# Kernel tuning notes

Measured on AMD Instinct MI355X. Metric: run time of the kernel, lower is better.

Reference implementation:

```python
import jax, jax.numpy as jnp
import numpy as np

H, D = 6, 64          # num_heads, head_dim (embed_dim = 384)
WIN = 33              # window_size
PAD = (WIN - 1) // 2  # 16


def setup_inputs() -> dict:
    key = jax.random.key(0)
    ks = jax.random.split(key, 9)
    B, L, E = 8, 1025, 384
    s = 1.0 / np.sqrt(E).astype(np.float32)
    return {
        "x": jax.random.normal(ks[0], (B, L, E), jnp.float32),
        "Wq": jax.random.normal(ks[1], (E, E), jnp.float32) * s,
        "bq": jax.random.normal(ks[2], (E,), jnp.float32) * 0.01,
        "Wk": jax.random.normal(ks[3], (E, E), jnp.float32) * s,
        "bk": jax.random.normal(ks[4], (E,), jnp.float32) * 0.01,
        "Wv": jax.random.normal(ks[5], (E, E), jnp.float32) * s,
        "bv": jax.random.normal(ks[6], (E,), jnp.float32) * 0.01,
        "Wo": jax.random.normal(ks[7], (E, E), jnp.float32) * s,
        "bo": jax.random.normal(ks[8], (E,), jnp.float32) * 0.01,
    }


def reference(x, Wq, bq, Wk, bk, Wv, bv, Wo, bo):
    B, L, E = x.shape
    scale = 1.0 / np.sqrt(D).astype(np.float32)

    def proj(W, b):
        # (B,L,E) -> (B,H,L,D)
        return (x @ W + b).reshape(B, L, H, D).transpose(0, 2, 1, 3)

    Q, K, V = proj(Wq, bq), proj(Wk, bk), proj(Wv, bv)

    # --- cls token (position 0): full attention over all keys ---
    s_cls = jnp.einsum('bhqd,bhkd->bhqk', Q[:, :, :1], K) * scale
    out_cls = jnp.einsum('bhqk,bhkd->bhqd', jax.nn.softmax(s_cls, -1), V)

    # --- remaining tokens: local window + cls appended to every window ---
    Lr = L - 1
    pos = jnp.arange(1, L)                                    # absolute query pos (Lr,)
    idx = pos[:, None] + jnp.arange(WIN)[None, :] - PAD
    # original masks out-of-range AND the cls slot (abs pos 0) inside the window
    valid = (idx >= 1) & (idx < L)
    idxc = jnp.clip(idx, 0, L - 1)

    Kw = K[:, :, idxc]
    Vw = V[:, :, idxc]
    cls_k = jnp.broadcast_to(K[:, :, :1, None, :], (B, H, Lr, 1, D))
    cls_v = jnp.broadcast_to(V[:, :, :1, None, :], (B, H, Lr, 1, D))
    Kw = jnp.concatenate([Kw, cls_k], axis=3)
    Vw = jnp.concatenate([Vw, cls_v], axis=3)
    mask = jnp.concatenate([valid, jnp.ones((Lr, 1), bool)], axis=-1)

    s_rest = jnp.einsum('bhld,bhlwd->bhlw', Q[:, :, 1:], Kw) * scale
    s_rest = jnp.where(mask[None, None], s_rest, -jnp.inf)
    a_rest = jax.nn.softmax(s_rest, axis=-1)
    out_rest = jnp.einsum('bhlw,bhlwd->bhld', a_rest, Vw)

    out = jnp.concatenate([out_cls, out_rest], axis=2)        # (B,H,L,D)
    out = out.transpose(0, 2, 1, 3).reshape(B, L, E)
    return out @ Wo + bo
```

## Files before the change

### kernel.cpp

```cpp
#include <hip/hip_runtime.h>
#include <hip/hip_bf16.h>

typedef unsigned short ushort_t;
typedef __attribute__((ext_vector_type(8))) short short8;
typedef __attribute__((ext_vector_type(4))) float f32x4;

constexpr int Bc = 8;
constexpr int Lc = 1025;
constexpr int Ec = 384;
constexpr int Hc = 6;
constexpr int Dc = 64;
constexpr int MT = Bc * Lc;
constexpr int BHLD = Bc * Hc * Lc * Dc;
constexpr int LT = 1032;
constexpr float SCALE = 0.125f;
constexpr int NCH = 5;

__device__ __forceinline__ float bf2f(ushort_t u) {
    union { unsigned int u; float f; } v; v.u = ((unsigned int)u) << 16; return v.f;
}
__device__ __forceinline__ ushort_t f2bf(float f) {
    union { float f; unsigned int u; } v; v.f = f;
    unsigned int r = v.u + 0x7FFFu + ((v.u >> 16) & 1u);
    return (ushort_t)(r >> 16);
}

#define GLOAD_LDS16(gp, lp)                                                          \
    __builtin_amdgcn_global_load_lds(                                                \
        (const __attribute__((address_space(1))) unsigned int*)(gp),                 \
        (__attribute__((address_space(3))) unsigned int*)(lp), 16, 0, 0)

__global__ __launch_bounds__(256) void cast_x_kernel(
    const float* __restrict__ x, ushort_t* __restrict__ xb)
{
    int i = blockIdx.x * 256 + threadIdx.x;
    float4 v = ((const float4*)x)[i];
    ushort4 o;
    o.x = f2bf(v.x); o.y = f2bf(v.y); o.z = f2bf(v.z); o.w = f2bf(v.w);
    ((ushort4*)xb)[i] = o;
}

__global__ __launch_bounds__(256) void castT_w_kernel(
    const float* __restrict__ Wq, const float* __restrict__ Wk,
    const float* __restrict__ Wv, const float* __restrict__ Wo,
    ushort_t* __restrict__ Wt_all)
{
    __shared__ float t[32][33];
    const int z = blockIdx.z;
    const float* W = (z == 0) ? Wq : (z == 1) ? Wk : (z == 2) ? Wv : Wo;
    ushort_t* Wt = Wt_all + (size_t)z * Ec * Ec;
    const int x0 = blockIdx.x * 32, y0 = blockIdx.y * 32;
    const int tx = threadIdx.x & 31, ty = threadIdx.x >> 5;
#pragma unroll
    for (int j = 0; j < 4; j++)
        t[ty + 8 * j][tx] = W[(size_t)(y0 + ty + 8 * j) * Ec + x0 + tx];
    __syncthreads();
#pragma unroll
    for (int j = 0; j < 4; j++)
        Wt[(size_t)(x0 + ty + 8 * j) * Ec + y0 + tx] = f2bf(t[tx][ty + 8 * j]);
}

__global__ __launch_bounds__(256) void qkv_mfma_kernel(
    const ushort_t* __restrict__ xb, const ushort_t* __restrict__ Wt,
    const float* __restrict__ bq, const float* __restrict__ bk,
    const float* __restrict__ bv, ushort_t* __restrict__ qkv)
{
    __shared__ __align__(16) ushort_t As[128 * 64];
    __shared__ __align__(16) ushort_t Bs[128 * 64];

    const int tid = threadIdx.x;
    const int lane = tid & 63;
    const int wid = tid >> 6;
    const int wr = wid >> 1, wc = wid & 1;
    const int m0 = blockIdx.x * 128;
    const int n0 = blockIdx.y * 128;
    const int which = n0 / Ec;
    const int nm0 = n0 - which * Ec;
    const ushort_t* Wmat = Wt + (size_t)which * Ec * Ec;
    const float* bias = (which == 0) ? bq : (which == 1) ? bk : bv;

    f32x4 acc[4][4];
#pragma unroll
    for (int i = 0; i < 4; i++)
#pragma unroll
        for (int j = 0; j < 4; j++) acc[i][j] = (f32x4){0.f, 0.f, 0.f, 0.f};

    for (int kt = 0; kt < Ec; kt += 64) {
#pragma unroll
        for (int c = 0; c < 4; c++) {
            int ci  = (wid * 4 + c) * 64 + lane;
            int row = ci >> 3, kc = ci & 7;
            int kcs = kc ^ (row & 7);
            int rowA = m0 + row; rowA = rowA < MT ? rowA : MT - 1;
            GLOAD_LDS16(xb + (size_t)rowA * Ec + kt + kcs * 8,
                        As + (size_t)(wid * 4 + c) * 512);
            GLOAD_LDS16(Wmat + (size_t)(nm0 + row) * Ec + kt + kcs * 8,
                        Bs + (size_t)(wid * 4 + c) * 512);
        }
        __syncthreads();

#pragma unroll
        for (int ki = 0; ki < 2; ki++) {
            short8 a[4], b[4];
            const int kchunk = ki * 4 + (lane >> 4);
#pragma unroll
            for (int mi = 0; mi < 4; mi++) {
                int row = wr * 64 + mi * 16 + (lane & 15);
                a[mi] = *(const short8*)(As + row * 64 + ((kchunk ^ (row & 7)) * 8));
            }
#pragma unroll
            for (int ni = 0; ni < 4; ni++) {
                int row = wc * 64 + ni * 16 + (lane & 15);
                b[ni] = *(const short8*)(Bs + row * 64 + ((kchunk ^ (row & 7)) * 8));
            }
#pragma unroll
            for (int mi = 0; mi < 4; mi++)
#pragma unroll
                for (int ni = 0; ni < 4; ni++)
                    acc[mi][ni] = __builtin_amdgcn_mfma_f32_16x16x32_bf16(
                        a[mi], b[ni], acc[mi][ni], 0, 0, 0);
        }
        __syncthreads();
    }

    const int colL = lane & 15;
    const int rowL = (lane >> 4) * 4;
#pragma unroll
    for (int ni = 0; ni < 4; ni++) {
        int nm = nm0 + wc * 64 + ni * 16 + colL;
        float bv_ = bias[nm];
        int h = nm >> 6, d = nm & 63;
#pragma unroll
        for (int mi = 0; mi < 4; mi++) {
#pragma unroll
            for (int r = 0; r < 4; r++) {
                int m = m0 + wr * 64 + mi * 16 + rowL + r;
                if (m < MT) {
                    int b_ = m / Lc, l = m - b_ * Lc;
                    qkv[(size_t)which * BHLD +
                        ((size_t)(b_ * Hc + h) * Lc + l) * Dc + d] =
                        f2bf(acc[mi][ni][r] + bv_);
                }
            }
        }
    }
}

__global__ __launch_bounds__(256) void vT_kernel(
    const ushort_t* __restrict__ qkv, ushort_t* __restrict__ vt)
{
    __shared__ ushort_t t[64][68];
    const int bh = blockIdx.y;
    const int l0 = blockIdx.x * 64;
    const ushort_t* V = qkv + 2 * (size_t)BHLD + (size_t)bh * Lc * Dc;
    ushort_t* vto = vt + (size_t)bh * 64 * LT;
    const int tid = threadIdx.x;
#pragma unroll
    for (int i = 0; i < 4; i++) {
        int idx = tid + i * 256;
        int l = idx >> 4, dc = idx & 15;
        int ls = l0 + l; ls = ls > 1024 ? 1024 : ls;
        ushort4 v = *(const ushort4*)(V + (size_t)ls * Dc + dc * 4);
        *(ushort4*)&t[l][dc * 4] = v;
    }
    __syncthreads();
#pragma unroll
    for (int i = 0; i < 4; i++) {
        int idx = tid + i * 256;
        int d = idx >> 4, lc = idx & 15;
        ushort4 o;
        o.x = t[lc * 4 + 0][d]; o.y = t[lc * 4 + 1][d];
        o.z = t[lc * 4 + 2][d]; o.w = t[lc * 4 + 3][d];
        int lw = l0 + lc * 4;
        if (lw <= 1024)
            *(ushort4*)(vto + (size_t)d * LT + lw) = o;
    }
}

__global__ __launch_bounds__(256) void cls_part_kernel(
    const ushort_t* __restrict__ qkv, float* __restrict__ part)
{
    const int bh = blockIdx.x, ch = blockIdx.y;
    const int base = ch * 256;
    const int count = min(256, Lc - base);
    const ushort_t* Q = qkv + (size_t)bh * Lc * Dc;
    const ushort_t* K = Q + (size_t)BHLD;
    const ushort_t* V = Q + 2 * (size_t)BHLD;

    __shared__ float qs[64];
    __shared__ float ps[256];
    __shared__ float red[256];

    const int tid = threadIdx.x;
    if (tid < 64) qs[tid] = bf2f(Q[tid]);
    __syncthreads();

    float s = -1e30f;
    if (tid < count) {
        const ushort4* kp = (const ushort4*)(K + (size_t)(base + tid) * Dc);
        float acc = 0.f;
#pragma unroll
        for (int c = 0; c < 16; c++) {
            ushort4 kv = kp[c];
            acc += qs[c * 4 + 0] * bf2f(kv.x) + qs[c * 4 + 1] * bf2f(kv.y) +
                   qs[c * 4 + 2] * bf2f(kv.z) + qs[c * 4 + 3] * bf2f(kv.w);
        }
        s = acc * SCALE;
    }
    red[tid] = s; __syncthreads();
    for (int off = 128; off > 0; off >>= 1) {
        if (tid < off) red[tid] = fmaxf(red[tid], red[tid + off]);
        __syncthreads();
    }
    const float m = red[0];
    __syncthreads();

    float p = (tid < count) ? __expf(s - m) : 0.f;
    ps[tid] = p;
    red[tid] = p; __syncthreads();
    for (int off = 128; off > 0; off >>= 1) {
        if (tid < off) red[tid] += red[tid + off];
        __syncthreads();
    }
    const float S = red[0];
    __syncthreads();

    const int d = tid & 63, sl = tid >> 6;
    float acc = 0.f;
    for (int i = sl; i < count; i += 4)
        acc += ps[i] * bf2f(V[(size_t)(base + i) * Dc + d]);
    red[tid] = acc; __syncthreads();
    if (tid < 64) {
        float o = red[tid] + red[tid + 64] + red[tid + 128] + red[tid + 192];
        float* pp = part + (size_t)(bh * NCH + ch) * 66;
        pp[2 + tid] = o;
        if (tid == 0) { pp[0] = m; pp[1] = S; }
    }
}

__global__ __launch_bounds__(64) void cls_comb_kernel(
    const float* __restrict__ part, ushort_t* __restrict__ attnb)
{
    const int bh = blockIdx.x, d = threadIdx.x;
    float M = -1e30f;
#pragma unroll
    for (int ch = 0; ch < NCH; ch++)
        M = fmaxf(M, part[(size_t)(bh * NCH + ch) * 66]);
    float S = 0.f, O = 0.f;
#pragma unroll
    for (int ch = 0; ch < NCH; ch++) {
        const float* pp = part + (size_t)(bh * NCH + ch) * 66;
        float w = __expf(pp[0] - M);
        S += pp[1] * w;
        O += pp[2 + d] * w;
    }
    const int b_ = bh / Hc, h = bh - b_ * Hc;
    attnb[(size_t)(b_ * Lc) * Ec + h * 64 + d] = f2bf(O / S);
}

__global__ __launch_bounds__(256) void win_mfma_kernel(
    const ushort_t* __restrict__ qkv, const ushort_t* __restrict__ vt,
    ushort_t* __restrict__ attnb)
{
    __shared__ __align__(16) ushort_t Kb[128 * 64];
    __shared__ __align__(16) ushort_t Vb[64 * 128];
    __shared__ __align__(16) ushort_t QP[64 * 128];

    const int t = blockIdx.x, bh = blockIdx.y;
    const int l0 = 1 + t * 64, k0 = l0 - 17;
    const int tid = threadIdx.x, lane = tid & 63, wid = tid >> 6;
    const ushort_t* Qg = qkv + (size_t)bh * Lc * Dc;
    const ushort_t* Kg = Qg + (size_t)BHLD;
    const ushort_t* Vt = vt + (size_t)bh * 64 * LT;

#pragma unroll
    for (int i = 0; i < 4; i++) {
        int p = (i * 4 + wid) * 64 + lane;
        {
            int j = p >> 3, c = p & 7, g = c ^ (j & 7);
            int kp = (j <= 111) ? min(max(k0 + j, 0), 1024) : 0;
            GLOAD_LDS16(Kg + (size_t)kp * Dc + g * 8,
                        Kb + (size_t)(i * 4 + wid) * 512);
        }
        {
            int d = p >> 4, jc = p & 15, g = jc ^ (d & 15);
            int kb = (g <= 13) ? max(k0 + g * 8, 0) : 0;
            GLOAD_LDS16(Vt + (size_t)d * LT + kb,
                        Vb + (size_t)(i * 4 + wid) * 512);
        }
    }
#pragma unroll
    for (int i = 0; i < 2; i++) {
        int p = (i * 4 + wid) * 64 + lane;
        int q = p >> 3, c = p & 7, g = c ^ (q & 7);
        GLOAD_LDS16(Qg + (size_t)(l0 + q) * Dc + g * 8,
                    QP + (size_t)(i * 4 + wid) * 512);
    }
    __syncthreads();

    f32x4 sacc[8];
#pragma unroll
    for (int tj = 0; tj < 8; tj++) sacc[tj] = (f32x4){0.f, 0.f, 0.f, 0.f};
#pragma unroll
    for (int ki = 0; ki < 2; ki++) {
        const int gc = ki * 4 + (lane >> 4);
        const int qrow = wid * 16 + (lane & 15);
        short8 a = *(const short8*)(QP + qrow * 64 + ((gc ^ (qrow & 7)) * 8));
#pragma unroll
        for (int tj = 0; tj < 8; tj++) {
            int jrow = tj * 16 + (lane & 15);
            short8 b = *(const short8*)(Kb + jrow * 64 + ((gc ^ (jrow & 7)) * 8));
            sacc[tj] = __builtin_amdgcn_mfma_f32_16x16x32_bf16(a, b, sacc[tj], 0, 0, 0);
        }
    }
    __syncthreads();

    const int qb = wid * 16 + (lane >> 4) * 4;
    const int cl = lane & 15;
    float inv[4];
#pragma unroll
    for (int r = 0; r < 4; r++) {
        const int q = qb + r;
        float sv[8];
        float mx = -1e30f;
#pragma unroll
        for (int tj = 0; tj < 8; tj++) {
            int j = tj * 16 + cl;
            int kp = k0 + j;
            bool valid = (j == 112) ||
                         ((j >= q + 1) && (j <= q + 33) && (kp >= 1) && (kp <= 1024));
            float s = valid ? sacc[tj][r] * SCALE : -1e30f;
            sv[tj] = s;
            mx = fmaxf(mx, s);
        }
        mx = fmaxf(mx, __shfl_xor(mx, 1));
        mx = fmaxf(mx, __shfl_xor(mx, 2));
        mx = fmaxf(mx, __shfl_xor(mx, 4));
        mx = fmaxf(mx, __shfl_xor(mx, 8));
        float sum = 0.f;
#pragma unroll
        for (int tj = 0; tj < 8; tj++) {
            float pv = __expf(sv[tj] - mx);
            sv[tj] = pv;
            sum += pv;
        }
        sum += __shfl_xor(sum, 1);
        sum += __shfl_xor(sum, 2);
        sum += __shfl_xor(sum, 4);
        sum += __shfl_xor(sum, 8);
        inv[r] = 1.f / sum;
#pragma unroll
        for (int tj = 0; tj < 8; tj++) {
            int j = tj * 16 + cl;
            QP[q * 128 + (((j >> 3) ^ (q & 15)) * 8) + (j & 7)] = f2bf(sv[tj]);
        }
    }
    __syncthreads();

    f32x4 oacc[4];
#pragma unroll
    for (int dt = 0; dt < 4; dt++) oacc[dt] = (f32x4){0.f, 0.f, 0.f, 0.f};
#pragma unroll
    for (int kc = 0; kc < 4; kc++) {
        const int gc = kc * 4 + (lane >> 4);
        const int qrow = wid * 16 + (lane & 15);
        short8 pa = *(const short8*)(QP + qrow * 128 + ((gc ^ (qrow & 15)) * 8));
#pragma unroll
        for (int dt = 0; dt < 4; dt++) {
            int drow = dt * 16 + (lane & 15);
            short8 vb = *(const short8*)(Vb + drow * 128 + ((gc ^ (drow & 15)) * 8));
            oacc[dt] = __builtin_amdgcn_mfma_f32_16x16x32_bf16(pa, vb, oacc[dt], 0, 0, 0);
        }
    }

    const int b_ = bh / Hc, h = bh - b_ * Hc;
#pragma unroll
    for (int dt = 0; dt < 4; dt++) {
        int d = dt * 16 + cl;
#pragma unroll
        for (int r = 0; r < 4; r++) {
            int l = l0 + qb + r;
            attnb[(size_t)(b_ * Lc + l) * Ec + h * 64 + d] = f2bf(oacc[dt][r] * inv[r]);
        }
    }
}

__global__ __launch_bounds__(256) void out_mfma_kernel(
    const ushort_t* __restrict__ attn_rows, const ushort_t* __restrict__ Wot,
    const float* __restrict__ bo, float* __restrict__ out)
{
    __shared__ __align__(16) ushort_t As[128 * 64];
    __shared__ __align__(16) ushort_t Bs[128 * 64];

    const int tid = threadIdx.x;
    const int lane = tid & 63;
    const int wid = tid >> 6;
    const int wr = wid >> 1, wc = wid & 1;
    const int m0 = blockIdx.x * 128;
    const int n0 = blockIdx.y * 128;

    f32x4 acc[4][4];
#pragma unroll
    for (int i = 0; i < 4; i++)
#pragma unroll
        for (int j = 0; j < 4; j++) acc[i][j] = (f32x4){0.f, 0.f, 0.f, 0.f};

    for (int kt = 0; kt < Ec; kt += 64) {
#pragma unroll
        for (int c = 0; c < 4; c++) {
            int ci  = (wid * 4 + c) * 64 + lane;
            int row = ci >> 3, kc = ci & 7;
            int kcs = kc ^ (row & 7);
            int rowA = m0 + row; rowA = rowA < MT ? rowA : MT - 1;
            GLOAD_LDS16(attn_rows + (size_t)rowA * Ec + kt + kcs * 8,
                        As + (size_t)(wid * 4 + c) * 512);
            GLOAD_LDS16(Wot + (size_t)(n0 + row) * Ec + kt + kcs * 8,
                        Bs + (size_t)(wid * 4 + c) * 512);
        }
        __syncthreads();

#pragma unroll
        for (int ki = 0; ki < 2; ki++) {
            short8 a[4], b[4];
            const int kchunk = ki * 4 + (lane >> 4);
#pragma unroll
            for (int mi = 0; mi < 4; mi++) {
                int row = wr * 64 + mi * 16 + (lane & 15);
                a[mi] = *(const short8*)(As + row * 64 + ((kchunk ^ (row & 7)) * 8));
            }
#pragma unroll
            for (int ni = 0; ni < 4; ni++) {
                int row = wc * 64 + ni * 16 + (lane & 15);
                b[ni] = *(const short8*)(Bs + row * 64 + ((kchunk ^ (row & 7)) * 8));
            }
#pragma unroll
            for (int mi = 0; mi < 4; mi++)
#pragma unroll
                for (int ni = 0; ni < 4; ni++)
                    acc[mi][ni] = __builtin_amdgcn_mfma_f32_16x16x32_bf16(
                        a[mi], b[ni], acc[mi][ni], 0, 0, 0);
        }
        __syncthreads();
    }

    const int colL = lane & 15;
    const int rowL = (lane >> 4) * 4;
#pragma unroll
    for (int ni = 0; ni < 4; ni++) {
        int n = n0 + wc * 64 + ni * 16 + colL;
        float bo_v = bo[n];
#pragma unroll
        for (int mi = 0; mi < 4; mi++) {
#pragma unroll
            for (int r = 0; r < 4; r++) {
                int m = m0 + wr * 64 + mi * 16 + rowL + r;
                if (m < MT) out[(size_t)m * Ec + n] = acc[mi][ni][r] + bo_v;
            }
        }
    }
}

extern "C" void kernel_launch(void* const* d_in, const int* in_sizes, int n_in,
                              void* d_out, int out_size, void* d_ws, size_t ws_size,
                              hipStream_t stream)
{
    const float* x  = (const float*)d_in[0];
    const float* Wq = (const float*)d_in[1];
    const float* bq = (const float*)d_in[2];
    const float* Wk = (const float*)d_in[3];
    const float* bk = (const float*)d_in[4];
    const float* Wv = (const float*)d_in[5];
    const float* bv = (const float*)d_in[6];
    const float* Wo = (const float*)d_in[7];
    const float* bo = (const float*)d_in[8];
    float* out = (float*)d_out;

    ushort_t* xb    = (ushort_t*)d_ws;
    ushort_t* Wt    = xb + (size_t)MT * Ec;
    ushort_t* qkvb  = Wt + (size_t)4 * Ec * Ec;
    ushort_t* vtb   = qkvb + (size_t)3 * BHLD;
    ushort_t* attnb = vtb + (size_t)Bc * Hc * 64 * LT;
    float* clsp     = (float*)(attnb + (size_t)MT * Ec);

    cast_x_kernel<<<(MT * Ec) / 4 / 256, 256, 0, stream>>>(x, xb);
    castT_w_kernel<<<dim3(12, 12, 4), 256, 0, stream>>>(Wq, Wk, Wv, Wo, Wt);

    qkv_mfma_kernel<<<dim3((MT + 127) / 128, 9), 256, 0, stream>>>(
        xb, Wt, bq, bk, bv, qkvb);

    vT_kernel<<<dim3(17, Bc * Hc), 256, 0, stream>>>(qkvb, vtb);

    cls_part_kernel<<<dim3(Bc * Hc, NCH), 256, 0, stream>>>(qkvb, clsp);
    cls_comb_kernel<<<Bc * Hc, 64, 0, stream>>>(clsp, attnb);

    win_mfma_kernel<<<dim3(16, Bc * Hc), 256, 0, stream>>>(qkvb, vtb, attnb);

    out_mfma_kernel<<<dim3((MT + 127) / 128, 3), 256, 0, stream>>>(
        attnb, Wt + (size_t)3 * Ec * Ec, bo, out);
}
```

Before: 175.5 us.

## Fuse cast kernels, fold cls attention into window kernel, shrink output GEMM tile

Merges the x cast and weight transpose-cast into one prep launch. The two-stage cls attention (partial plus combine) becomes one extra block per head inside the window attention kernel, computed by a single block over all 1025 keys. The output projection GEMM M-tile drops from 128 to 64 rows, doubling block count for better occupancy on the large CU count. Together these cut three kernel launches, but the cls work is now a serial single-block tail per head.

```diff
diff --git a/kernel.cpp b/kernel.cpp
--- a/kernel.cpp
+++ b/kernel.cpp
@@ -14,7 +14,6 @@
 constexpr int BHLD = Bc * Hc * Lc * Dc;
 constexpr int LT = 1032;
 constexpr float SCALE = 0.125f;
-constexpr int NCH = 5;
 
 __device__ __forceinline__ float bf2f(ushort_t u) {
     union { unsigned int u; float f; } v; v.u = ((unsigned int)u) << 16; return v.f;
@@ -30,26 +29,28 @@
         (const __attribute__((address_space(1))) unsigned int*)(gp),                 \
         (__attribute__((address_space(3))) unsigned int*)(lp), 16, 0, 0)
 
-__global__ __launch_bounds__(256) void cast_x_kernel(
-    const float* __restrict__ x, ushort_t* __restrict__ xb)
-{
-    int i = blockIdx.x * 256 + threadIdx.x;
-    float4 v = ((const float4*)x)[i];
-    ushort4 o;
-    o.x = f2bf(v.x); o.y = f2bf(v.y); o.z = f2bf(v.z); o.w = f2bf(v.w);
-    ((ushort4*)xb)[i] = o;
-}
-
-__global__ __launch_bounds__(256) void castT_w_kernel(
+__global__ __launch_bounds__(256) void prep_kernel(
+    const float* __restrict__ x, ushort_t* __restrict__ xb,
     const float* __restrict__ Wq, const float* __restrict__ Wk,
     const float* __restrict__ Wv, const float* __restrict__ Wo,
     ushort_t* __restrict__ Wt_all)
 {
+    const int bid = blockIdx.x;
+    if (bid < 3075) {
+        int i = bid * 256 + threadIdx.x;
+        float4 v = ((const float4*)x)[i];
+        ushort4 o;
+        o.x = f2bf(v.x); o.y = f2bf(v.y); o.z = f2bf(v.z); o.w = f2bf(v.w);
+        ((ushort4*)xb)[i] = o;
+        return;
+    }
     __shared__ float t[32][33];
-    const int z = blockIdx.z;
+    const int b2 = bid - 3075;
+    const int z = b2 / 144, rem = b2 - z * 144;
+    const int yy = rem / 12, xx = rem - yy * 12;
     const float* W = (z == 0) ? Wq : (z == 1) ? Wk : (z == 2) ? Wv : Wo;
     ushort_t* Wt = Wt_all + (size_t)z * Ec * Ec;
-    const int x0 = blockIdx.x * 32, y0 = blockIdx.y * 32;
+    const int x0 = xx * 32, y0 = yy * 32;
     const int tx = threadIdx.x & 31, ty = threadIdx.x >> 5;
 #pragma unroll
     for (int j = 0; j < 4; j++)
@@ -177,88 +178,7 @@
     }
 }
 
-__global__ __launch_bounds__(256) void cls_part_kernel(
-    const ushort_t* __restrict__ qkv, float* __restrict__ part)
-{
-    const int bh = blockIdx.x, ch = blockIdx.y;
-    const int base = ch * 256;
-    const int count = min(256, Lc - base);
-    const ushort_t* Q = qkv + (size_t)bh * Lc * Dc;
-    const ushort_t* K = Q + (size_t)BHLD;
-    const ushort_t* V = Q + 2 * (size_t)BHLD;
-
-    __shared__ float qs[64];
-    __shared__ float ps[256];
-    __shared__ float red[256];
-
-    const int tid = threadIdx.x;
-    if (tid < 64) qs[tid] = bf2f(Q[tid]);
-    __syncthreads();
-
-    float s = -1e30f;
-    if (tid < count) {
-        const ushort4* kp = (const ushort4*)(K + (size_t)(base + tid) * Dc);
-        float acc = 0.f;
-#pragma unroll
-        for (int c = 0; c < 16; c++) {
-            ushort4 kv = kp[c];
-            acc += qs[c * 4 + 0] * bf2f(kv.x) + qs[c * 4 + 1] * bf2f(kv.y) +
-                   qs[c * 4 + 2] * bf2f(kv.z) + qs[c * 4 + 3] * bf2f(kv.w);
-        }
-        s = acc * SCALE;
-    }
-    red[tid] = s; __syncthreads();
-    for (int off = 128; off > 0; off >>= 1) {
-        if (tid < off) red[tid] = fmaxf(red[tid], red[tid + off]);
-        __syncthreads();
-    }
-    const float m = red[0];
-    __syncthreads();
-
-    float p = (tid < count) ? __expf(s - m) : 0.f;
-    ps[tid] = p;
-    red[tid] = p; __syncthreads();
-    for (int off = 128; off > 0; off >>= 1) {
-        if (tid < off) red[tid] += red[tid + off];
-        __syncthreads();
-    }
-    const float S = red[0];
-    __syncthreads();
-
-    const int d = tid & 63, sl = tid >> 6;
-    float acc = 0.f;
-    for (int i = sl; i < count; i += 4)
-        acc += ps[i] * bf2f(V[(size_t)(base + i) * Dc + d]);
-    red[tid] = acc; __syncthreads();
-    if (tid < 64) {
-        float o = red[tid] + red[tid + 64] + red[tid + 128] + red[tid + 192];
-        float* pp = part + (size_t)(bh * NCH + ch) * 66;
-        pp[2 + tid] = o;
-        if (tid == 0) { pp[0] = m; pp[1] = S; }
-    }
-}
-
-__global__ __launch_bounds__(64) void cls_comb_kernel(
-    const float* __restrict__ part, ushort_t* __restrict__ attnb)
-{
-    const int bh = blockIdx.x, d = threadIdx.x;
-    float M = -1e30f;
-#pragma unroll
-    for (int ch = 0; ch < NCH; ch++)
-        M = fmaxf(M, part[(size_t)(bh * NCH + ch) * 66]);
-    float S = 0.f, O = 0.f;
-#pragma unroll
-    for (int ch = 0; ch < NCH; ch++) {
-        const float* pp = part + (size_t)(bh * NCH + ch) * 66;
-        float w = __expf(pp[0] - M);
-        S += pp[1] * w;
-        O += pp[2 + d] * w;
-    }
-    const int b_ = bh / Hc, h = bh - b_ * Hc;
-    attnb[(size_t)(b_ * Lc) * Ec + h * 64 + d] = f2bf(O / S);
-}
-
-__global__ __launch_bounds__(256) void win_mfma_kernel(
+__global__ __launch_bounds__(256) void attn_kernel(
     const ushort_t* __restrict__ qkv, const ushort_t* __restrict__ vt,
     ushort_t* __restrict__ attnb)
 {
@@ -266,11 +186,71 @@
     __shared__ __align__(16) ushort_t Vb[64 * 128];
     __shared__ __align__(16) ushort_t QP[64 * 128];
 
-    const int t = blockIdx.x, bh = blockIdx.y;
-    const int l0 = 1 + t * 64, k0 = l0 - 17;
+    const int bh = blockIdx.y;
     const int tid = threadIdx.x, lane = tid & 63, wid = tid >> 6;
     const ushort_t* Qg = qkv + (size_t)bh * Lc * Dc;
     const ushort_t* Kg = Qg + (size_t)BHLD;
+    const int b_ = bh / Hc, h = bh - b_ * Hc;
+
+    if (blockIdx.x == 16) {
+        const ushort_t* Vg = Qg + 2 * (size_t)BHLD;
+        float* sc  = (float*)Kb;
+        float* red = (float*)Vb;
+
+        unsigned int qw = ((const unsigned int*)Qg)[lane & 31];
+        float qa = bf2f((ushort_t)(qw & 0xffff)), qb = bf2f((ushort_t)(qw >> 16));
+
+        float lmax = -1e30f;
+        for (int s = 0; s < 129; ++s) {
+            int k = s * 8 + wid * 2 + (lane >> 5);
+            bool ok = k < Lc;
+            int kc = ok ? k : 0;
+            unsigned int kw = ((const unsigned int*)(Kg + (size_t)kc * Dc))[lane & 31];
+            float p = qa * bf2f((ushort_t)(kw & 0xffff)) +
+                      qb * bf2f((ushort_t)(kw >> 16));
+            p += __shfl_xor(p, 1);  p += __shfl_xor(p, 2);
+            p += __shfl_xor(p, 4);  p += __shfl_xor(p, 8);
+            p += __shfl_xor(p, 16);
+            float s0 = p * SCALE;
+            if (ok && (lane & 31) == 0) sc[k] = s0;
+            float so = __shfl_xor(s0, 32);
+            int ko = s * 8 + wid * 2 + 1 - (lane >> 5);
+            if (!ok) s0 = -1e30f;
+            if (ko >= Lc) so = -1e30f;
+            lmax = fmaxf(lmax, fmaxf(s0, so));
+        }
+        if (lane == 0) red[wid] = lmax;
+        __syncthreads();
+        const float M = fmaxf(fmaxf(red[0], red[1]), fmaxf(red[2], red[3]));
+
+        float lsum = 0.f;
+        for (int k = tid; k < Lc; k += 256) {
+            float p = __expf(sc[k] - M);
+            sc[k] = p;
+            lsum += p;
+        }
+        lsum += __shfl_xor(lsum, 1);  lsum += __shfl_xor(lsum, 2);
+        lsum += __shfl_xor(lsum, 4);  lsum += __shfl_xor(lsum, 8);
+        lsum += __shfl_xor(lsum, 16); lsum += __shfl_xor(lsum, 32);
+        __syncthreads();
+        if (lane == 0) red[8 + wid] = lsum;
+        __syncthreads();
+        const float S = red[8] + red[9] + red[10] + red[11];
+
+        float acc = 0.f;
+        for (int k = wid; k < Lc; k += 4)
+            acc += sc[k] * bf2f(Vg[(size_t)k * Dc + lane]);
+        red[64 + wid * 64 + lane] = acc;
+        __syncthreads();
+        if (tid < 64) {
+            float o = red[64 + tid] + red[128 + tid] + red[192 + tid] + red[256 + tid];
+            attnb[(size_t)(b_ * Lc) * Ec + h * 64 + tid] = f2bf(o / S);
+        }
+        return;
+    }
+
+    const int t = blockIdx.x;
+    const int l0 = 1 + t * 64, k0 = l0 - 17;
     const ushort_t* Vt = vt + (size_t)bh * 64 * LT;
 
 #pragma unroll
@@ -373,7 +353,6 @@
         }
     }
 
-    const int b_ = bh / Hc, h = bh - b_ * Hc;
 #pragma unroll
     for (int dt = 0; dt < 4; dt++) {
         int d = dt * 16 + cl;
@@ -389,31 +368,37 @@
     const ushort_t* __restrict__ attn_rows, const ushort_t* __restrict__ Wot,
     const float* __restrict__ bo, float* __restrict__ out)
 {
-    __shared__ __align__(16) ushort_t As[128 * 64];
+    __shared__ __align__(16) ushort_t As[64 * 64];
     __shared__ __align__(16) ushort_t Bs[128 * 64];
 
     const int tid = threadIdx.x;
     const int lane = tid & 63;
     const int wid = tid >> 6;
-    const int wr = wid >> 1, wc = wid & 1;
-    const int m0 = blockIdx.x * 128;
+    const int wr = wid & 1, wc = wid >> 1;
+    const int m0 = blockIdx.x * 64;
     const int n0 = blockIdx.y * 128;
 
-    f32x4 acc[4][4];
-#pragma unroll
-    for (int i = 0; i < 4; i++)
+    f32x4 acc[2][4];
+#pragma unroll
+    for (int i = 0; i < 2; i++)
 #pragma unroll
         for (int j = 0; j < 4; j++) acc[i][j] = (f32x4){0.f, 0.f, 0.f, 0.f};
 
     for (int kt = 0; kt < Ec; kt += 64) {
+#pragma unroll
+        for (int c = 0; c < 2; c++) {
+            int ci  = (wid * 2 + c) * 64 + lane;
+            int row = ci >> 3, kc = ci & 7;
+            int kcs = kc ^ (row & 7);
+            int rowA = m0 + row; rowA = rowA < MT ? rowA : MT - 1;
+            GLOAD_LDS16(attn_rows + (size_t)rowA * Ec + kt + kcs * 8,
+                        As + (size_t)(wid * 2 + c) * 512);
+        }
 #pragma unroll
         for (int c = 0; c < 4; c++) {
             int ci  = (wid * 4 + c) * 64 + lane;
             int row = ci >> 3, kc = ci & 7;
             int kcs = kc ^ (row & 7);
-            int rowA = m0 + row; rowA = rowA < MT ? rowA : MT - 1;
-            GLOAD_LDS16(attn_rows + (size_t)rowA * Ec + kt + kcs * 8,
-                        As + (size_t)(wid * 4 + c) * 512);
             GLOAD_LDS16(Wot + (size_t)(n0 + row) * Ec + kt + kcs * 8,
                         Bs + (size_t)(wid * 4 + c) * 512);
         }
@@ -421,11 +406,11 @@
 
 #pragma unroll
         for (int ki = 0; ki < 2; ki++) {
-            short8 a[4], b[4];
+            short8 a[2], b[4];
             const int kchunk = ki * 4 + (lane >> 4);
 #pragma unroll
-            for (int mi = 0; mi < 4; mi++) {
-                int row = wr * 64 + mi * 16 + (lane & 15);
+            for (int mi = 0; mi < 2; mi++) {
+                int row = wr * 32 + mi * 16 + (lane & 15);
                 a[mi] = *(const short8*)(As + row * 64 + ((kchunk ^ (row & 7)) * 8));
             }
 #pragma unroll
@@ -434,7 +419,7 @@
                 b[ni] = *(const short8*)(Bs + row * 64 + ((kchunk ^ (row & 7)) * 8));
             }
 #pragma unroll
-            for (int mi = 0; mi < 4; mi++)
+            for (int mi = 0; mi < 2; mi++)
 #pragma unroll
                 for (int ni = 0; ni < 4; ni++)
                     acc[mi][ni] = __builtin_amdgcn_mfma_f32_16x16x32_bf16(
@@ -450,10 +435,10 @@
         int n = n0 + wc * 64 + ni * 16 + colL;
         float bo_v = bo[n];
 #pragma unroll
-        for (int mi = 0; mi < 4; mi++) {
+        for (int mi = 0; mi < 2; mi++) {
 #pragma unroll
             for (int r = 0; r < 4; r++) {
-                int m = m0 + wr * 64 + mi * 16 + rowL + r;
+                int m = m0 + wr * 32 + mi * 16 + rowL + r;
                 if (m < MT) out[(size_t)m * Ec + n] = acc[mi][ni][r] + bo_v;
             }
         }
@@ -480,21 +465,16 @@
     ushort_t* qkvb  = Wt + (size_t)4 * Ec * Ec;
     ushort_t* vtb   = qkvb + (size_t)3 * BHLD;
     ushort_t* attnb = vtb + (size_t)Bc * Hc * 64 * LT;
-    float* clsp     = (float*)(attnb + (size_t)MT * Ec);
-
-    cast_x_kernel<<<(MT * Ec) / 4 / 256, 256, 0, stream>>>(x, xb);
-    castT_w_kernel<<<dim3(12, 12, 4), 256, 0, stream>>>(Wq, Wk, Wv, Wo, Wt);
+
+    prep_kernel<<<3075 + 576, 256, 0, stream>>>(x, xb, Wq, Wk, Wv, Wo, Wt);
 
     qkv_mfma_kernel<<<dim3((MT + 127) / 128, 9), 256, 0, stream>>>(
         xb, Wt, bq, bk, bv, qkvb);
 
     vT_kernel<<<dim3(17, Bc * Hc), 256, 0, stream>>>(qkvb, vtb);
 
-    cls_part_kernel<<<dim3(Bc * Hc, NCH), 256, 0, stream>>>(qkvb, clsp);
-    cls_comb_kernel<<<Bc * Hc, 64, 0, stream>>>(clsp, attnb);
-
-    win_mfma_kernel<<<dim3(16, Bc * Hc), 256, 0, stream>>>(qkvb, vtb, attnb);
-
-    out_mfma_kernel<<<dim3((MT + 127) / 128, 3), 256, 0, stream>>>(
+    attn_kernel<<<dim3(17, Bc * Hc), 256, 0, stream>>>(qkvb, vtb, attnb);
+
+    out_mfma_kernel<<<dim3((MT + 63) / 64, 3), 256, 0, stream>>>(
         attnb, Wt + (size_t)3 * Ec * Ec, bo, out);
 }
```

New measurement: 270.3 us. 54.0% more time.

## Merge small kernels into fewer launches and shrink out-projection M tile

Applied to the files above, without the earlier changes.

Folds the x cast and weight transpose-cast into one prep kernel, merges the V transpose with the cls partial attention, and folds the cls combine into an extra block column of the window attention kernel. The goal is fewer kernel launches and less inter-kernel idle time. The out-projection GEMM also moves from 128x128 to 64x128 tiles, doubling its grid to fill more CUs at the cost of reloading the Wo tile more often. Merged kernels take on the largest shared-memory footprint of any branch, which may lower occupancy for the lighter branches.

```diff
diff --git a/kernel.cpp b/kernel.cpp
--- a/kernel.cpp
+++ b/kernel.cpp
@@ -30,26 +30,28 @@
         (const __attribute__((address_space(1))) unsigned int*)(gp),                 \
         (__attribute__((address_space(3))) unsigned int*)(lp), 16, 0, 0)
 
-__global__ __launch_bounds__(256) void cast_x_kernel(
-    const float* __restrict__ x, ushort_t* __restrict__ xb)
-{
-    int i = blockIdx.x * 256 + threadIdx.x;
-    float4 v = ((const float4*)x)[i];
-    ushort4 o;
-    o.x = f2bf(v.x); o.y = f2bf(v.y); o.z = f2bf(v.z); o.w = f2bf(v.w);
-    ((ushort4*)xb)[i] = o;
-}
-
-__global__ __launch_bounds__(256) void castT_w_kernel(
+__global__ __launch_bounds__(256) void prep_kernel(
+    const float* __restrict__ x, ushort_t* __restrict__ xb,
     const float* __restrict__ Wq, const float* __restrict__ Wk,
     const float* __restrict__ Wv, const float* __restrict__ Wo,
     ushort_t* __restrict__ Wt_all)
 {
+    const int bid = blockIdx.x;
+    if (bid < 3075) {
+        int i = bid * 256 + threadIdx.x;
+        float4 v = ((const float4*)x)[i];
+        ushort4 o;
+        o.x = f2bf(v.x); o.y = f2bf(v.y); o.z = f2bf(v.z); o.w = f2bf(v.w);
+        ((ushort4*)xb)[i] = o;
+        return;
+    }
     __shared__ float t[32][33];
-    const int z = blockIdx.z;
+    const int b2 = bid - 3075;
+    const int z = b2 / 144, rem = b2 - z * 144;
+    const int yy = rem / 12, xx = rem - yy * 12;
     const float* W = (z == 0) ? Wq : (z == 1) ? Wk : (z == 2) ? Wv : Wo;
     ushort_t* Wt = Wt_all + (size_t)z * Ec * Ec;
-    const int x0 = blockIdx.x * 32, y0 = blockIdx.y * 32;
+    const int x0 = xx * 32, y0 = yy * 32;
     const int tx = threadIdx.x & 31, ty = threadIdx.x >> 5;
 #pragma unroll
     for (int j = 0; j < 4; j++)
@@ -146,52 +148,52 @@
     }
 }
 
-__global__ __launch_bounds__(256) void vT_kernel(
-    const ushort_t* __restrict__ qkv, ushort_t* __restrict__ vt)
+__global__ __launch_bounds__(256) void vt_cls_kernel(
+    const ushort_t* __restrict__ qkv, ushort_t* __restrict__ vt,
+    float* __restrict__ part)
 {
-    __shared__ ushort_t t[64][68];
     const int bh = blockIdx.y;
-    const int l0 = blockIdx.x * 64;
-    const ushort_t* V = qkv + 2 * (size_t)BHLD + (size_t)bh * Lc * Dc;
-    ushort_t* vto = vt + (size_t)bh * 64 * LT;
     const int tid = threadIdx.x;
-#pragma unroll
-    for (int i = 0; i < 4; i++) {
-        int idx = tid + i * 256;
-        int l = idx >> 4, dc = idx & 15;
-        int ls = l0 + l; ls = ls > 1024 ? 1024 : ls;
-        ushort4 v = *(const ushort4*)(V + (size_t)ls * Dc + dc * 4);
-        *(ushort4*)&t[l][dc * 4] = v;
-    }
-    __syncthreads();
-#pragma unroll
-    for (int i = 0; i < 4; i++) {
-        int idx = tid + i * 256;
-        int d = idx >> 4, lc = idx & 15;
-        ushort4 o;
-        o.x = t[lc * 4 + 0][d]; o.y = t[lc * 4 + 1][d];
-        o.z = t[lc * 4 + 2][d]; o.w = t[lc * 4 + 3][d];
-        int lw = l0 + lc * 4;
-        if (lw <= 1024)
-            *(ushort4*)(vto + (size_t)d * LT + lw) = o;
-    }
-}
-
-__global__ __launch_bounds__(256) void cls_part_kernel(
-    const ushort_t* __restrict__ qkv, float* __restrict__ part)
-{
-    const int bh = blockIdx.x, ch = blockIdx.y;
+
+    if (blockIdx.x < 17) {
+        __shared__ ushort_t t[64][68];
+        const int l0 = blockIdx.x * 64;
+        const ushort_t* V = qkv + 2 * (size_t)BHLD + (size_t)bh * Lc * Dc;
+        ushort_t* vto = vt + (size_t)bh * 64 * LT;
+#pragma unroll
+        for (int i = 0; i < 4; i++) {
+            int idx = tid + i * 256;
+            int l = idx >> 4, dc = idx & 15;
+            int ls = l0 + l; ls = ls > 1024 ? 1024 : ls;
+            ushort4 v = *(const ushort4*)(V + (size_t)ls * Dc + dc * 4);
+            *(ushort4*)&t[l][dc * 4] = v;
+        }
+        __syncthreads();
+#pragma unroll
+        for (int i = 0; i < 4; i++) {
+            int idx = tid + i * 256;
+            int d = idx >> 4, lc = idx & 15;
+            ushort4 o;
+            o.x = t[lc * 4 + 0][d]; o.y = t[lc * 4 + 1][d];
+            o.z = t[lc * 4 + 2][d]; o.w = t[lc * 4 + 3][d];
+            int lw = l0 + lc * 4;
+            if (lw <= 1024)
+                *(ushort4*)(vto + (size_t)d * LT + lw) = o;
+        }
+        return;
+    }
+
+    __shared__ float qs[64];
+    __shared__ float ps[256];
+    __shared__ float red[256];
+
+    const int ch = blockIdx.x - 17;
     const int base = ch * 256;
     const int count = min(256, Lc - base);
     const ushort_t* Q = qkv + (size_t)bh * Lc * Dc;
     const ushort_t* K = Q + (size_t)BHLD;
     const ushort_t* V = Q + 2 * (size_t)BHLD;
 
-    __shared__ float qs[64];
-    __shared__ float ps[256];
-    __shared__ float red[256];
-
-    const int tid = threadIdx.x;
     if (tid < 64) qs[tid] = bf2f(Q[tid]);
     __syncthreads();
 
@@ -238,37 +240,38 @@
     }
 }
 
-__global__ __launch_bounds__(64) void cls_comb_kernel(
+__global__ __launch_bounds__(256) void win_attn_kernel(
+    const ushort_t* __restrict__ qkv, const ushort_t* __restrict__ vt,
     const float* __restrict__ part, ushort_t* __restrict__ attnb)
-{
-    const int bh = blockIdx.x, d = threadIdx.x;
-    float M = -1e30f;
-#pragma unroll
-    for (int ch = 0; ch < NCH; ch++)
-        M = fmaxf(M, part[(size_t)(bh * NCH + ch) * 66]);
-    float S = 0.f, O = 0.f;
-#pragma unroll
-    for (int ch = 0; ch < NCH; ch++) {
-        const float* pp = part + (size_t)(bh * NCH + ch) * 66;
-        float w = __expf(pp[0] - M);
-        S += pp[1] * w;
-        O += pp[2 + d] * w;
-    }
-    const int b_ = bh / Hc, h = bh - b_ * Hc;
-    attnb[(size_t)(b_ * Lc) * Ec + h * 64 + d] = f2bf(O / S);
-}
-
-__global__ __launch_bounds__(256) void win_mfma_kernel(
-    const ushort_t* __restrict__ qkv, const ushort_t* __restrict__ vt,
-    ushort_t* __restrict__ attnb)
 {
     __shared__ __align__(16) ushort_t Kb[128 * 64];
     __shared__ __align__(16) ushort_t Vb[64 * 128];
     __shared__ __align__(16) ushort_t QP[64 * 128];
 
-    const int t = blockIdx.x, bh = blockIdx.y;
+    const int bh = blockIdx.y;
+    const int tid = threadIdx.x, lane = tid & 63, wid = tid >> 6;
+    const int b_ = bh / Hc, h = bh - b_ * Hc;
+
+    if (blockIdx.x == 16) {
+        if (tid >= 64) return;
+        float M = -1e30f;
+#pragma unroll
+        for (int ch = 0; ch < NCH; ch++)
+            M = fmaxf(M, part[(size_t)(bh * NCH + ch) * 66]);
+        float S = 0.f, O = 0.f;
+#pragma unroll
+        for (int ch = 0; ch < NCH; ch++) {
+            const float* pp = part + (size_t)(bh * NCH + ch) * 66;
+            float w = __expf(pp[0] - M);
+            S += pp[1] * w;
+            O += pp[2 + tid] * w;
+        }
+        attnb[(size_t)(b_ * Lc) * Ec + h * 64 + tid] = f2bf(O / S);
+        return;
+    }
+
+    const int t = blockIdx.x;
     const int l0 = 1 + t * 64, k0 = l0 - 17;
-    const int tid = threadIdx.x, lane = tid & 63, wid = tid >> 6;
     const ushort_t* Qg = qkv + (size_t)bh * Lc * Dc;
     const ushort_t* Kg = Qg + (size_t)BHLD;
     const ushort_t* Vt = vt + (size_t)bh * 64 * LT;
@@ -373,7 +376,6 @@
         }
     }
 
-    const int b_ = bh / Hc, h = bh - b_ * Hc;
 #pragma unroll
     for (int dt = 0; dt < 4; dt++) {
         int d = dt * 16 + cl;
@@ -389,31 +391,37 @@
     const ushort_t* __restrict__ attn_rows, const ushort_t* __restrict__ Wot,
     const float* __restrict__ bo, float* __restrict__ out)
 {
-    __shared__ __align__(16) ushort_t As[128 * 64];
+    __shared__ __align__(16) ushort_t As[64 * 64];
     __shared__ __align__(16) ushort_t Bs[128 * 64];
 
     const int tid = threadIdx.x;
     const int lane = tid & 63;
     const int wid = tid >> 6;
-    const int wr = wid >> 1, wc = wid & 1;
-    const int m0 = blockIdx.x * 128;
+    const int wr = wid & 1, wc = wid >> 1;
+    const int m0 = blockIdx.x * 64;
     const int n0 = blockIdx.y * 128;
 
-    f32x4 acc[4][4];
-#pragma unroll
-    for (int i = 0; i < 4; i++)
+    f32x4 acc[2][4];
+#pragma unroll
+    for (int i = 0; i < 2; i++)
 #pragma unroll
         for (int j = 0; j < 4; j++) acc[i][j] = (f32x4){0.f, 0.f, 0.f, 0.f};
 
     for (int kt = 0; kt < Ec; kt += 64) {
+#pragma unroll
+        for (int c = 0; c < 2; c++) {
+            int ci  = (wid * 2 + c) * 64 + lane;
+            int row = ci >> 3, kc = ci & 7;
+            int kcs = kc ^ (row & 7);
+            int rowA = m0 + row; rowA = rowA < MT ? rowA : MT - 1;
+            GLOAD_LDS16(attn_rows + (size_t)rowA * Ec + kt + kcs * 8,
+                        As + (size_t)(wid * 2 + c) * 512);
+        }
 #pragma unroll
         for (int c = 0; c < 4; c++) {
             int ci  = (wid * 4 + c) * 64 + lane;
             int row = ci >> 3, kc = ci & 7;
             int kcs = kc ^ (row & 7);
-            int rowA = m0 + row; rowA = rowA < MT ? rowA : MT - 1;
-            GLOAD_LDS16(attn_rows + (size_t)rowA * Ec + kt + kcs * 8,
-                        As + (size_t)(wid * 4 + c) * 512);
             GLOAD_LDS16(Wot + (size_t)(n0 + row) * Ec + kt + kcs * 8,
                         Bs + (size_t)(wid * 4 + c) * 512);
         }
@@ -421,11 +429,11 @@
 
 #pragma unroll
         for (int ki = 0; ki < 2; ki++) {
-            short8 a[4], b[4];
+            short8 a[2], b[4];
             const int kchunk = ki * 4 + (lane >> 4);
 #pragma unroll
-            for (int mi = 0; mi < 4; mi++) {
-                int row = wr * 64 + mi * 16 + (lane & 15);
+            for (int mi = 0; mi < 2; mi++) {
+                int row = wr * 32 + mi * 16 + (lane & 15);
                 a[mi] = *(const short8*)(As + row * 64 + ((kchunk ^ (row & 7)) * 8));
             }
 #pragma unroll
@@ -434,7 +442,7 @@
                 b[ni] = *(const short8*)(Bs + row * 64 + ((kchunk ^ (row & 7)) * 8));
             }
 #pragma unroll
-            for (int mi = 0; mi < 4; mi++)
+            for (int mi = 0; mi < 2; mi++)
 #pragma unroll
                 for (int ni = 0; ni < 4; ni++)
                     acc[mi][ni] = __builtin_amdgcn_mfma_f32_16x16x32_bf16(
@@ -450,10 +458,10 @@
         int n = n0 + wc * 64 + ni * 16 + colL;
         float bo_v = bo[n];
 #pragma unroll
-        for (int mi = 0; mi < 4; mi++) {
+        for (int mi = 0; mi < 2; mi++) {
 #pragma unroll
             for (int r = 0; r < 4; r++) {
-                int m = m0 + wr * 64 + mi * 16 + rowL + r;
+                int m = m0 + wr * 32 + mi * 16 + rowL + r;
                 if (m < MT) out[(size_t)m * Ec + n] = acc[mi][ni][r] + bo_v;
             }
         }
@@ -482,19 +490,15 @@
     ushort_t* attnb = vtb + (size_t)Bc * Hc * 64 * LT;
     float* clsp     = (float*)(attnb + (size_t)MT * Ec);
 
-    cast_x_kernel<<<(MT * Ec) / 4 / 256, 256, 0, stream>>>(x, xb);
-    castT_w_kernel<<<dim3(12, 12, 4), 256, 0, stream>>>(Wq, Wk, Wv, Wo, Wt);
+    prep_kernel<<<3075 + 576, 256, 0, stream>>>(x, xb, Wq, Wk, Wv, Wo, Wt);
 
     qkv_mfma_kernel<<<dim3((MT + 127) / 128, 9), 256, 0, stream>>>(
         xb, Wt, bq, bk, bv, qkvb);
 
-    vT_kernel<<<dim3(17, Bc * Hc), 256, 0, stream>>>(qkvb, vtb);
-
-    cls_part_kernel<<<dim3(Bc * Hc, NCH), 256, 0, stream>>>(qkvb, clsp);
-    cls_comb_kernel<<<Bc * Hc, 64, 0, stream>>>(clsp, attnb);
-
-    win_mfma_kernel<<<dim3(16, Bc * Hc), 256, 0, stream>>>(qkvb, vtb, attnb);
-
-    out_mfma_kernel<<<dim3((MT + 127) / 128, 3), 256, 0, stream>>>(
+    vt_cls_kernel<<<dim3(17 + NCH, Bc * Hc), 256, 0, stream>>>(qkvb, vtb, clsp);
+
+    win_attn_kernel<<<dim3(17, Bc * Hc), 256, 0, stream>>>(qkvb, vtb, clsp, attnb);
+
+    out_mfma_kernel<<<dim3((MT + 63) / 64, 3), 256, 0, stream>>>(
         attnb, Wt + (size_t)3 * Ec * Ec, bo, out);
 }
```

Result: faster. 165.2 us (-5.9%).
